# Performance work log

Measured on AMD Instinct MI355X. Metric: run time of the kernel, lower is better.

Reference implementation:

```python
import jax, jax.numpy as jnp
import numpy as np

# Static tree structure: B jets, each a perfect binary tree of depth DEPTH.
B = 64
DEPTH = 12                       # levels 0..DEPTH; level j has B*2**j nodes
N_FEAT = 7
N_HID = 128
LEVEL_SIZES = [B * (1 << j) for j in range(DEPTH + 1)]
OFFSETS = np.concatenate([[0], np.cumsum(LEVEL_SIZES)]).astype(np.int64).tolist()
TOTAL = OFFSETS[-1]              # 524224 nodes
INNER_SIZES = LEVEL_SIZES[:-1]   # all nodes inner except leaf level
INNER_OFF = np.concatenate([[0], np.cumsum(INNER_SIZES)]).astype(np.int64).tolist()


def setup_inputs() -> dict:
    key = jax.random.key(0)
    k_c, k_wu, k_wh = jax.random.split(key, 3)
    contents = jax.random.normal(k_c, (TOTAL, N_FEAT), dtype=jnp.float32)
    # children: per level j < DEPTH, a random pairing (permutation) of level j+1 nodes
    rng = np.random.default_rng(0)
    ch = []
    for j in range(DEPTH):
        perm = rng.permutation(LEVEL_SIZES[j + 1]).astype(np.int32)
        ch.append(perm.reshape(LEVEL_SIZES[j], 2))
    children = jnp.asarray(np.concatenate(ch, axis=0))  # [262080, 2]
    # Learned params (torch nn.Linear: y = x @ W.T + b)
    w_u = jax.random.normal(k_wu, (N_HID, N_FEAT), dtype=jnp.float32) / np.float32(np.sqrt(N_FEAT))
    b_u = jnp.zeros((N_HID,), jnp.float32)
    w_h = jax.random.normal(k_wh, (N_HID, 3 * N_HID), dtype=jnp.float32) / np.float32(np.sqrt(3 * N_HID))
    b_h = jnp.zeros((N_HID,), jnp.float32)
    return {"contents": contents, "children": children,
            "w_u": w_u, "b_u": b_u, "w_h": w_h, "b_h": b_h}


def reference(contents, children, w_u, b_u, w_h, b_h):
    # Bottom-up pass over tree levels (leaves -> root), mirroring the torch loop
    # over levels[::-1]. Perfect binary tree: every non-leaf node is inner.
    emb = None
    for j in range(DEPTH, -1, -1):
        c_j = contents[OFFSETS[j]:OFFSETS[j + 1]]              # [B*2^j, F]
        u = jnp.tanh(c_j @ w_u.T + b_u)                        # [B*2^j, H]
        if j < DEPTH:
            ch_j = children[INNER_OFF[j]:INNER_OFF[j + 1]]     # [B*2^j, 2]
            h_L = emb[ch_j[:, 0]]                              # gather from prev level
            h_R = emb[ch_j[:, 1]]
            emb = jnp.tanh(jnp.concatenate([h_L, h_R, u], axis=1) @ w_h.T + b_h)
        else:
            emb = u  # leaf level: no inner nodes
    return emb.reshape(B, -1)  # root embedding per jet: [B, N_HID]
```

## Files before the change

kernel.cpp:

```cpp
#include <hip/hip_runtime.h>
#include <hip/hip_bf16.h>


#define NF 7
#define NH 128
#define NLEAF 262144
#define XSTR 136
#define XSTR3 392

typedef __bf16 bf16;
typedef __bf16 bf16x8 __attribute__((ext_vector_type(8)));
typedef float floatx16 __attribute__((ext_vector_type(16)));

__device__ __forceinline__ float ftanh(float x){
    float e = __expf(2.0f * x);
    return 1.0f - __fdividef(2.0f, e + 1.0f);
}

__global__ __launch_bounds__(256) void k_leaf(
    const float* __restrict__ contents, const int2* __restrict__ children,
    const float* __restrict__ w_u, const float* __restrict__ b_u,
    const float* __restrict__ w_h,
    unsigned int* __restrict__ embA_u32, unsigned int* __restrict__ usm_u32,
    bf16* __restrict__ wb, int* __restrict__ ids_A, int* __restrict__ ids_B)
{
    const int t = threadIdx.x;
    const int b = blockIdx.x;

    if (b >= 2560){
        if (b < 2564){
            int root = (b - 2560) * 256 + t;
            int* base = ids_A + root * 128;
            const int2* ch4 = children + 960;
            const int2* ch5 = children + 1984;
            const int2* ch6 = children + 4032;
            const int2* ch7 = children + 8128;
            const int2* ch8 = children + 16320;
            const int2* ch9 = children + 32704;
            int l5[2], l6[4], l7[8], l8[16], l9[32];
            { int2 c = ch4[root]; l5[0] = c.x; l5[1] = c.y; }
            #pragma unroll
            for (int k = 0; k < 2; ++k){ int2 c = ch5[l5[k]]; l6[2*k] = c.x; l6[2*k+1] = c.y; }
            #pragma unroll
            for (int k = 0; k < 4; ++k){ int2 c = ch6[l6[k]]; l7[2*k] = c.x; l7[2*k+1] = c.y; }
            #pragma unroll
            for (int k = 0; k < 8; ++k){ int2 c = ch7[l7[k]]; l8[2*k] = c.x; l8[2*k+1] = c.y; }
            #pragma unroll
            for (int k = 0; k < 16; ++k){ int2 c = ch8[l8[k]]; l9[2*k] = c.x; l9[2*k+1] = c.y; }
            base[0] = root;
            base[1] = l5[0]; base[2] = l5[1];
            #pragma unroll
            for (int k = 0; k < 4; ++k)  base[3 + k]  = l6[k];
            #pragma unroll
            for (int k = 0; k < 8; ++k)  base[7 + k]  = l7[k];
            #pragma unroll
            for (int k = 0; k < 16; ++k) base[15 + k] = l8[k];
            #pragma unroll
            for (int k = 0; k < 32; ++k) base[31 + k] = l9[k];
            #pragma unroll
            for (int k = 0; k < 32; ++k){
                int2 c = ch9[l9[k]];
                base[63 + 2*k] = c.x; base[64 + 2*k] = c.y;
            }
        } else if (t < 64){
            int root = t;
            int* base = ids_B + root * 32;
            const int2* ch0 = children;
            const int2* ch1 = children + 64;
            const int2* ch2 = children + 192;
            const int2* ch3 = children + 448;
            int l1[2], l2[4], l3[8];
            { int2 c = ch0[root]; l1[0] = c.x; l1[1] = c.y; }
            #pragma unroll
            for (int k = 0; k < 2; ++k){ int2 c = ch1[l1[k]]; l2[2*k] = c.x; l2[2*k+1] = c.y; }
            #pragma unroll
            for (int k = 0; k < 4; ++k){ int2 c = ch2[l2[k]]; l3[2*k] = c.x; l3[2*k+1] = c.y; }
            base[0] = root;
            base[1] = l1[0]; base[2] = l1[1];
            #pragma unroll
            for (int k = 0; k < 4; ++k) base[3 + k] = l2[k];
            #pragma unroll
            for (int k = 0; k < 8; ++k) base[7 + k] = l3[k];
            #pragma unroll
            for (int k = 0; k < 8; ++k){
                int2 c = ch3[l3[k]];
                base[15 + 2*k] = c.x; base[16 + 2*k] = c.y;
            }
        }
        return;
    }

    __shared__ float csL[128 * 8];
    if (b < 192) wb[b * 256 + t] = (bf16)w_h[b * 256 + t];

    const int leaf = (b < 2048);
    const size_t srow = leaf ? (262080 + (size_t)b * 128) : ((size_t)(b - 2048) * 128);
    unsigned int* dst = leaf ? embA_u32 : usm_u32;
    const size_t drow = leaf ? ((size_t)b * 128) : ((size_t)(b - 2048) * 128);

    if (t < 224){
        float4 v = ((const float4*)(contents + srow * NF))[t];
        int e = t * 4;
        float vv[4] = {v.x, v.y, v.z, v.w};
        #pragma unroll
        for (int r = 0; r < 4; ++r){ int ee = e + r; csL[(ee/7)*8 + (ee%7)] = vv[r]; }
    }
    const int cp = t & 63;
    const int quarter = t >> 6;
    float wu0[NF], wu1[NF];
    const float* w0 = w_u + (size_t)(2 * cp) * NF;
    #pragma unroll
    for (int f = 0; f < NF; ++f){ wu0[f] = w0[f]; wu1[f] = w0[NF + f]; }
    const float bu0 = b_u[2 * cp], bu1 = b_u[2 * cp + 1];
    __syncthreads();
    #pragma unroll 4
    for (int i = 0; i < 32; ++i){
        int node = quarter * 32 + i;
        float4 c0 = *(const float4*)&csL[node * 8];
        float4 c1 = *(const float4*)&csL[node * 8 + 4];
        float a0 = bu0, a1 = bu1;
        a0 = fmaf(c0.x, wu0[0], a0); a1 = fmaf(c0.x, wu1[0], a1);
        a0 = fmaf(c0.y, wu0[1], a0); a1 = fmaf(c0.y, wu1[1], a1);
        a0 = fmaf(c0.z, wu0[2], a0); a1 = fmaf(c0.z, wu1[2], a1);
        a0 = fmaf(c0.w, wu0[3], a0); a1 = fmaf(c0.w, wu1[3], a1);
        a0 = fmaf(c1.x, wu0[4], a0); a1 = fmaf(c1.x, wu1[4], a1);
        a0 = fmaf(c1.y, wu0[5], a0); a1 = fmaf(c1.y, wu1[5], a1);
        a0 = fmaf(c1.z, wu0[6], a0); a1 = fmaf(c1.z, wu1[6], a1);
        union { unsigned int u; bf16 h[2]; } pk;
        pk.h[0] = (bf16)ftanh(a0);
        pk.h[1] = (bf16)ftanh(a1);
        dst[(drow + node) * 64 + cp] = pk.u;
    }
}

__global__ __launch_bounds__(256, 4) void k_inner(
    const int2* __restrict__ children, const float* __restrict__ contents,
    const float* __restrict__ w_u, const float* __restrict__ b_u,
    const bf16* __restrict__ wb, const float* __restrict__ b_h,
    const bf16* __restrict__ emb_next, bf16* __restrict__ out_b)
{
    __shared__ bf16 xs[64 * XSTR];
    __shared__ int2 ch_s[64];
    __shared__ float cs[64 * 8];
    const int t = threadIdx.x;
    const int block0 = blockIdx.x * 64;
    if (t < 64) ch_s[t] = children[block0 + t];
    if (t < 112){
        float4 v = ((const float4*)(contents + (size_t)block0 * NF))[t];
        int e = t * 4;
        float vv[4] = {v.x, v.y, v.z, v.w};
        #pragma unroll
        for (int r = 0; r < 4; ++r){ int ee = e + r; cs[(ee/7)*8 + (ee%7)] = vv[r]; }
    }
    const int cp = t & 63;
    const int quarter = t >> 6;
    float wu0[NF], wu1[NF];
    {
        const float* w0 = w_u + (size_t)(2 * cp) * NF;
        #pragma unroll
        for (int f = 0; f < NF; ++f){ wu0[f] = w0[f]; wu1[f] = w0[NF + f]; }
    }
    const float bu0 = b_u[2 * cp], bu1 = b_u[2 * cp + 1];
    const int lane = t & 63;
    const int ct = t >> 6;
    const int m = lane & 31;
    const int q = lane >> 5;
    floatx16 acc0 = {0,0,0,0,0,0,0,0,0,0,0,0,0,0,0,0};
    floatx16 acc1 = {0,0,0,0,0,0,0,0,0,0,0,0,0,0,0,0};
    const bf16* bq = wb + ((size_t)(ct * 32 + m) * 384 + q * 8);
    #pragma unroll 1
    for (int p = 0; p < 3; ++p){
        __syncthreads();
        if (p < 2){
            #pragma unroll
            for (int r = 0; r < 4; ++r){
                int task = r * 256 + t;
                int i = task >> 4, part = task & 15;
                int row = (p == 0) ? ch_s[i].x : ch_s[i].y;
                uint4 v = *(const uint4*)(emb_next + (size_t)row * NH + part * 8);
                *(uint4*)&xs[i * XSTR + part * 8] = v;
            }
        } else {
            #pragma unroll 4
            for (int i = 0; i < 16; ++i){
                int node = quarter * 16 + i;
                float4 c0 = *(const float4*)&cs[node * 8];
                float4 c1 = *(const float4*)&cs[node * 8 + 4];
                float a0 = bu0, a1 = bu1;
                a0 = fmaf(c0.x, wu0[0], a0); a1 = fmaf(c0.x, wu1[0], a1);
                a0 = fmaf(c0.y, wu0[1], a0); a1 = fmaf(c0.y, wu1[1], a1);
                a0 = fmaf(c0.z, wu0[2], a0); a1 = fmaf(c0.z, wu1[2], a1);
                a0 = fmaf(c0.w, wu0[3], a0); a1 = fmaf(c0.w, wu1[3], a1);
                a0 = fmaf(c1.x, wu0[4], a0); a1 = fmaf(c1.x, wu1[4], a1);
                a0 = fmaf(c1.y, wu0[5], a0); a1 = fmaf(c1.y, wu1[5], a1);
                a0 = fmaf(c1.z, wu0[6], a0); a1 = fmaf(c1.z, wu1[6], a1);
                union { unsigned int u; bf16 h[2]; } pk;
                pk.h[0] = (bf16)ftanh(a0);
                pk.h[1] = (bf16)ftanh(a1);
                ((unsigned int*)xs)[node * (XSTR / 2) + cp] = pk.u;
            }
        }
        bf16x8 bfr[8];
        #pragma unroll
        for (int kk = 0; kk < 8; ++kk)
            bfr[kk] = *(const bf16x8*)(bq + p * 128 + kk * 16);
        __syncthreads();
        const bf16* xa = &xs[m * XSTR + q * 8];
        #pragma unroll
        for (int kk = 0; kk < 8; ++kk){
            bf16x8 a0 = *(const bf16x8*)(xa + kk * 16);
            bf16x8 a1 = *(const bf16x8*)(xa + kk * 16 + 32 * XSTR);
            acc0 = __builtin_amdgcn_mfma_f32_32x32x16_bf16(a0, bfr[kk], acc0, 0, 0, 0);
            acc1 = __builtin_amdgcn_mfma_f32_32x32x16_bf16(a1, bfr[kk], acc1, 0, 0, 0);
        }
    }
    const int colg = ct * 32 + m;
    const float bv = b_h[colg];
    #pragma unroll
    for (int nt = 0; nt < 2; ++nt){
        const floatx16* accp = nt ? &acc1 : &acc0;
        #pragma unroll
        for (int r = 0; r < 16; ++r){
            int row  = (r & 3) + 8 * (r >> 2) + 4 * q;
            int node = block0 + nt * 32 + row;
            out_b[(size_t)node * NH + colg] = (bf16)ftanh((*accp)[r] + bv);
        }
    }
}

__global__ __launch_bounds__(256, 2) void k_tailA(
    const int* __restrict__ ids_A, const bf16* __restrict__ u_small,
    const bf16* __restrict__ wb, const float* __restrict__ b_h,
    const bf16* __restrict__ emb10, bf16* __restrict__ emb4)
{
    __shared__ bf16 xs[32 * XSTR3];
    __shared__ bf16 embL[32 * 136];
    __shared__ int ids[128];
    const int t = threadIdx.x, root = blockIdx.x;
    const int ct = t >> 6, lane = t & 63, m = lane & 31, q = lane >> 5;
    const float bv = b_h[ct * 32 + m];
    if (t < 32) ((uint4*)ids)[t] = ((const uint4*)(ids_A + root * 128))[t];
    __syncthreads();
    const bf16* bq = wb + ((size_t)(ct * 32 + m) * 384 + q * 8);

    #pragma unroll 1
    for (int l = 9; l >= 4; --l){
        const int n = 1 << (l - 4);
        #pragma unroll 1
        for (int r = 0; r < 4; ++r){
            int task = r * 256 + t;
            if (task < n * 32){
                int i = task >> 5, half = (task >> 4) & 1, part = task & 15;
                uint4 v;
                if (l == 9) v = *(const uint4*)(emb10 + (size_t)ids[63 + 2*i + half] * NH + part * 8);
                else        v = *(uint4*)&embL[(2*i + half) * 136 + part * 8];
                *(uint4*)&xs[i * XSTR3 + half * 128 + part * 8] = v;
            }
        }
        #pragma unroll 1
        for (int r = 0; r < 2; ++r){
            int task = r * 256 + t;
            if (task < n * 16){
                int i = task >> 4, part = task & 15;
                size_t row = (size_t)64 * ((1u << l) - 1) + ids[(n - 1) + i];
                *(uint4*)&xs[i * XSTR3 + 256 + part * 8] =
                    *(const uint4*)(u_small + row * NH + part * 8);
            }
        }
        __syncthreads();
        floatx16 accs[3];
        #pragma unroll
        for (int g = 0; g < 3; ++g) accs[g] = (floatx16){0,0,0,0,0,0,0,0,0,0,0,0,0,0,0,0};
        const bf16* xa = &xs[m * XSTR3 + q * 8];
        #pragma unroll
        for (int grp = 0; grp < 3; ++grp){
            bf16x8 bfr[8];
            #pragma unroll
            for (int kk = 0; kk < 8; ++kk)
                bfr[kk] = *(const bf16x8*)(bq + grp * 128 + kk * 16);
            #pragma unroll
            for (int kk = 0; kk < 8; ++kk){
                bf16x8 a0 = *(const bf16x8*)(xa + grp * 128 + kk * 16);
                accs[grp] = __builtin_amdgcn_mfma_f32_32x32x16_bf16(a0, bfr[kk], accs[grp], 0, 0, 0);
            }
        }
        floatx16 acc = accs[0] + accs[1] + accs[2];
        __syncthreads();
        #pragma unroll
        for (int r = 0; r < 16; ++r){
            int row = (r & 3) + 8 * (r >> 2) + 4 * q;
            if (row < n){
                float v = ftanh(acc[r] + bv);
                if (l > 4) embL[row * 136 + ct * 32 + m] = (bf16)v;
                else       emb4[(size_t)root * NH + ct * 32 + m] = (bf16)v;
            }
        }
        __syncthreads();
    }
}

__global__ __launch_bounds__(256, 2) void k_tailB(
    const int* __restrict__ ids_B, const bf16* __restrict__ u_small,
    const bf16* __restrict__ wb, const float* __restrict__ b_h,
    const bf16* __restrict__ emb4, float* __restrict__ out_f)
{
    __shared__ bf16 xs[8 * XSTR3];
    __shared__ bf16 embL[8 * 136];
    __shared__ int ids[32];
    const int t = threadIdx.x, root = blockIdx.x;
    const int ct = t >> 6, lane = t & 63, m = lane & 31, q = lane >> 5;
    const float bv = b_h[ct * 32 + m];
    if (t < 8) ((uint4*)ids)[t] = ((const uint4*)(ids_B + root * 32))[t];
    __syncthreads();
    const bf16* bq = wb + ((size_t)(ct * 32 + m) * 384 + q * 8);

    #pragma unroll 1
    for (int l = 3; l >= 0; --l){
        const int n = 1 << l;
        {
            int task = t;
            if (task < n * 32){
                int i = task >> 5, half = (task >> 4) & 1, part = task & 15;
                uint4 v;
                if (l == 3) v = *(const uint4*)(emb4 + (size_t)ids[15 + 2*i + half] * NH + part * 8);
                else        v = *(uint4*)&embL[(2*i + half) * 136 + part * 8];
                *(uint4*)&xs[i * XSTR3 + half * 128 + part * 8] = v;
            }
            if (task < n * 16){
                int i = task >> 4, part = task & 15;
                size_t row = (size_t)64 * ((1u << l) - 1) + ids[(n - 1) + i];
                *(uint4*)&xs[i * XSTR3 + 256 + part * 8] =
                    *(const uint4*)(u_small + row * NH + part * 8);
            }
        }
        __syncthreads();
        floatx16 accs[3];
        #pragma unroll
        for (int g = 0; g < 3; ++g) accs[g] = (floatx16){0,0,0,0,0,0,0,0,0,0,0,0,0,0,0,0};
        const bf16* xa = &xs[m * XSTR3 + q * 8];
        #pragma unroll
        for (int grp = 0; grp < 3; ++grp){
            bf16x8 bfr[8];
            #pragma unroll
            for (int kk = 0; kk < 8; ++kk)
                bfr[kk] = *(const bf16x8*)(bq + grp * 128 + kk * 16);
            #pragma unroll
            for (int kk = 0; kk < 8; ++kk){
                bf16x8 a0 = *(const bf16x8*)(xa + grp * 128 + kk * 16);
                accs[grp] = __builtin_amdgcn_mfma_f32_32x32x16_bf16(a0, bfr[kk], accs[grp], 0, 0, 0);
            }
        }
        floatx16 acc = accs[0] + accs[1] + accs[2];
        __syncthreads();
        #pragma unroll
        for (int r = 0; r < 16; ++r){
            int row = (r & 3) + 8 * (r >> 2) + 4 * q;
            if (row < n){
                float v = ftanh(acc[r] + bv);
                if (l > 0) embL[row * 136 + ct * 32 + m] = (bf16)v;
                else       out_f[(size_t)root * NH + ct * 32 + m] = v;
            }
        }
        __syncthreads();
    }
}

extern "C" void kernel_launch(void* const* d_in, const int* in_sizes, int n_in,
                              void* d_out, int out_size, void* d_ws, size_t ws_size,
                              hipStream_t stream){
    const float* contents = (const float*)d_in[0];
    const int2*  children = (const int2*)d_in[1];
    const float* w_u      = (const float*)d_in[2];
    const float* b_u      = (const float*)d_in[3];
    const float* w_h      = (const float*)d_in[4];
    const float* b_h      = (const float*)d_in[5];
    float* outf = (float*)d_out;

    bf16* embA    = (bf16*)d_ws;
    bf16* embB    = embA + (size_t)NLEAF * NH;
    bf16* wb      = embB + (size_t)131072 * NH;
    bf16* u_small = wb + (size_t)NH * 384;
    int*  ids_A   = (int*)(u_small + (size_t)65536 * NH);
    int*  ids_B   = ids_A + 1024 * 128;

    hipLaunchKernelGGL(k_leaf, dim3(2565), dim3(256), 0, stream,
                       contents, children, w_u, b_u, w_h,
                       (unsigned int*)embA, (unsigned int*)u_small, wb, ids_A, ids_B);
    hipLaunchKernelGGL(k_inner, dim3(2048), dim3(256), 0, stream,
                       children + 131008, contents + (size_t)131008 * NF,
                       w_u, b_u, wb, b_h, embA, embB);
    hipLaunchKernelGGL(k_inner, dim3(1024), dim3(256), 0, stream,
                       children + 65472, contents + (size_t)65472 * NF,
                       w_u, b_u, wb, b_h, embB, embA);
    hipLaunchKernelGGL(k_tailA, dim3(1024), dim3(256), 0, stream,
                       ids_A, u_small, wb, b_h, embA, embB);
    hipLaunchKernelGGL(k_tailB, dim3(64), dim3(256), 0, stream,
                       ids_B, u_small, wb, b_h, embB, outf);
}
```

Measured before the change: 229.8 us.

## Fuse leaf embedding into level-11 inner kernel, skipping leaf-embedding round trip

The leaf level's tanh(Wu·x) is now computed on the fly inside a new level-11 kernel. Each block gathers its children's leaf contents directly, builds the leaf and node embeddings in shared memory, and runs the MFMA combine. This removes the full leaf-embedding write and re-gather through global memory (about 64 MB of bf16 traffic) and one kernel launch. In exchange, each block reads w_h in fp32 and converts it to bf16 itself rather than using the precomputed wb, which is still built by tail blocks. It also uses more shared memory per block and limits occupancy to two blocks per CU.

After: 240.4 us. 4.6% more time.

```diff
diff --git a/kernel.cpp b/kernel.cpp
--- a/kernel.cpp
+++ b/kernel.cpp
@@ -4,7 +4,6 @@
 
 #define NF 7
 #define NH 128
-#define NLEAF 262144
 #define XSTR 136
 #define XSTR3 392
 
@@ -17,18 +16,58 @@
     return 1.0f - __fdividef(2.0f, e + 1.0f);
 }
 
-__global__ __launch_bounds__(256) void k_leaf(
+__global__ __launch_bounds__(256, 2) void k_lvl11(
     const float* __restrict__ contents, const int2* __restrict__ children,
     const float* __restrict__ w_u, const float* __restrict__ b_u,
-    const float* __restrict__ w_h,
-    unsigned int* __restrict__ embA_u32, unsigned int* __restrict__ usm_u32,
-    bf16* __restrict__ wb, int* __restrict__ ids_A, int* __restrict__ ids_B)
+    const float* __restrict__ w_h, const float* __restrict__ b_h,
+    bf16* __restrict__ emb11,
+    unsigned int* __restrict__ usm_u32, int* __restrict__ ids_A,
+    int* __restrict__ ids_B, bf16* __restrict__ wb)
 {
+    __shared__ bf16 xs[64 * XSTR3];
+    __shared__ float cs2[128 * 8];
+    __shared__ float cs[64 * 8];
+    __shared__ int chS[128];
     const int t = threadIdx.x;
     const int b = blockIdx.x;
 
-    if (b >= 2560){
-        if (b < 2564){
+    if (b >= 2048){
+        if (b < 2560){
+            const size_t srow = (size_t)(b - 2048) * 128;
+            if (t < 224){
+                float4 v = ((const float4*)(contents + srow * NF))[t];
+                int e = t * 4;
+                float vv[4] = {v.x, v.y, v.z, v.w};
+                #pragma unroll
+                for (int r = 0; r < 4; ++r){ int ee = e + r; cs2[(ee/7)*8 + (ee%7)] = vv[r]; }
+            }
+            const int cp = t & 63;
+            const int quarter = t >> 6;
+            float wu0[NF], wu1[NF];
+            const float* w0 = w_u + (size_t)(2 * cp) * NF;
+            #pragma unroll
+            for (int f = 0; f < NF; ++f){ wu0[f] = w0[f]; wu1[f] = w0[NF + f]; }
+            const float bu0 = b_u[2 * cp], bu1 = b_u[2 * cp + 1];
+            __syncthreads();
+            #pragma unroll 4
+            for (int i = 0; i < 32; ++i){
+                int node = quarter * 32 + i;
+                float4 c0 = *(const float4*)&cs2[node * 8];
+                float4 c1 = *(const float4*)&cs2[node * 8 + 4];
+                float a0 = bu0, a1 = bu1;
+                a0 = fmaf(c0.x, wu0[0], a0); a1 = fmaf(c0.x, wu1[0], a1);
+                a0 = fmaf(c0.y, wu0[1], a0); a1 = fmaf(c0.y, wu1[1], a1);
+                a0 = fmaf(c0.z, wu0[2], a0); a1 = fmaf(c0.z, wu1[2], a1);
+                a0 = fmaf(c0.w, wu0[3], a0); a1 = fmaf(c0.w, wu1[3], a1);
+                a0 = fmaf(c1.x, wu0[4], a0); a1 = fmaf(c1.x, wu1[4], a1);
+                a0 = fmaf(c1.y, wu0[5], a0); a1 = fmaf(c1.y, wu1[5], a1);
+                a0 = fmaf(c1.z, wu0[6], a0); a1 = fmaf(c1.z, wu1[6], a1);
+                union { unsigned int u; bf16 h[2]; } pk;
+                pk.h[0] = (bf16)ftanh(a0);
+                pk.h[1] = (bf16)ftanh(a1);
+                usm_u32[(srow + node) * 64 + cp] = pk.u;
+            }
+        } else if (b < 2564){
             int root = (b - 2560) * 256 + t;
             int* base = ids_A + root * 128;
             const int2* ch4 = children + 960;
@@ -62,62 +101,78 @@
                 int2 c = ch9[l9[k]];
                 base[63 + 2*k] = c.x; base[64 + 2*k] = c.y;
             }
-        } else if (t < 64){
-            int root = t;
-            int* base = ids_B + root * 32;
-            const int2* ch0 = children;
-            const int2* ch1 = children + 64;
-            const int2* ch2 = children + 192;
-            const int2* ch3 = children + 448;
-            int l1[2], l2[4], l3[8];
-            { int2 c = ch0[root]; l1[0] = c.x; l1[1] = c.y; }
-            #pragma unroll
-            for (int k = 0; k < 2; ++k){ int2 c = ch1[l1[k]]; l2[2*k] = c.x; l2[2*k+1] = c.y; }
-            #pragma unroll
-            for (int k = 0; k < 4; ++k){ int2 c = ch2[l2[k]]; l3[2*k] = c.x; l3[2*k+1] = c.y; }
-            base[0] = root;
-            base[1] = l1[0]; base[2] = l1[1];
-            #pragma unroll
-            for (int k = 0; k < 4; ++k) base[3 + k] = l2[k];
-            #pragma unroll
-            for (int k = 0; k < 8; ++k) base[7 + k] = l3[k];
-            #pragma unroll
-            for (int k = 0; k < 8; ++k){
-                int2 c = ch3[l3[k]];
-                base[15 + 2*k] = c.x; base[16 + 2*k] = c.y;
-            }
+        } else if (b == 2564){
+            if (t < 64){
+                int root = t;
+                int* base = ids_B + root * 32;
+                const int2* ch0 = children;
+                const int2* ch1 = children + 64;
+                const int2* ch2 = children + 192;
+                const int2* ch3 = children + 448;
+                int l1[2], l2[4], l3[8];
+                { int2 c = ch0[root]; l1[0] = c.x; l1[1] = c.y; }
+                #pragma unroll
+                for (int k = 0; k < 2; ++k){ int2 c = ch1[l1[k]]; l2[2*k] = c.x; l2[2*k+1] = c.y; }
+                #pragma unroll
+                for (int k = 0; k < 4; ++k){ int2 c = ch2[l2[k]]; l3[2*k] = c.x; l3[2*k+1] = c.y; }
+                base[0] = root;
+                base[1] = l1[0]; base[2] = l1[1];
+                #pragma unroll
+                for (int k = 0; k < 4; ++k) base[3 + k] = l2[k];
+                #pragma unroll
+                for (int k = 0; k < 8; ++k) base[7 + k] = l3[k];
+                #pragma unroll
+                for (int k = 0; k < 8; ++k){
+                    int2 c = ch3[l3[k]];
+                    base[15 + 2*k] = c.x; base[16 + 2*k] = c.y;
+                }
+            }
+        } else {
+            int idx = (b - 2565) * 256 + t;
+            wb[idx] = (bf16)w_h[idx];
         }
         return;
     }
 
-    __shared__ float csL[128 * 8];
-    if (b < 192) wb[b * 256 + t] = (bf16)w_h[b * 256 + t];
-
-    const int leaf = (b < 2048);
-    const size_t srow = leaf ? (262080 + (size_t)b * 128) : ((size_t)(b - 2048) * 128);
-    unsigned int* dst = leaf ? embA_u32 : usm_u32;
-    const size_t drow = leaf ? ((size_t)b * 128) : ((size_t)(b - 2048) * 128);
-
-    if (t < 224){
-        float4 v = ((const float4*)(contents + srow * NF))[t];
+    const int node0 = b * 64;
+    const int2* ch11 = children + 131008;
+    const float* cont11 = contents + (size_t)131008 * NF;
+    const float* contL  = contents + (size_t)262080 * NF;
+
+    if (t < 64){ int2 c = ch11[node0 + t]; chS[2*t] = c.x; chS[2*t + 1] = c.y; }
+    if (t < 112){
+        float4 v = ((const float4*)(cont11 + (size_t)node0 * NF))[t];
         int e = t * 4;
         float vv[4] = {v.x, v.y, v.z, v.w};
         #pragma unroll
-        for (int r = 0; r < 4; ++r){ int ee = e + r; csL[(ee/7)*8 + (ee%7)] = vv[r]; }
-    }
+        for (int r = 0; r < 4; ++r){ int ee = e + r; cs[(ee/7)*8 + (ee%7)] = vv[r]; }
+    }
+
     const int cp = t & 63;
     const int quarter = t >> 6;
     float wu0[NF], wu1[NF];
-    const float* w0 = w_u + (size_t)(2 * cp) * NF;
-    #pragma unroll
-    for (int f = 0; f < NF; ++f){ wu0[f] = w0[f]; wu1[f] = w0[NF + f]; }
+    {
+        const float* w0 = w_u + (size_t)(2 * cp) * NF;
+        #pragma unroll
+        for (int f = 0; f < NF; ++f){ wu0[f] = w0[f]; wu1[f] = w0[NF + f]; }
+    }
     const float bu0 = b_u[2 * cp], bu1 = b_u[2 * cp + 1];
+    unsigned int* xs32 = (unsigned int*)xs;
+
     __syncthreads();
+
+    float c7[NF];
+    if (t < 128){
+        const float* src = contL + (size_t)chS[t] * NF;
+        #pragma unroll
+        for (int f = 0; f < NF; ++f) c7[f] = src[f];
+    }
+
     #pragma unroll 4
-    for (int i = 0; i < 32; ++i){
-        int node = quarter * 32 + i;
-        float4 c0 = *(const float4*)&csL[node * 8];
-        float4 c1 = *(const float4*)&csL[node * 8 + 4];
+    for (int k = 0; k < 16; ++k){
+        int i = quarter * 16 + k;
+        float4 c0 = *(const float4*)&cs[i * 8];
+        float4 c1 = *(const float4*)&cs[i * 8 + 4];
         float a0 = bu0, a1 = bu1;
         a0 = fmaf(c0.x, wu0[0], a0); a1 = fmaf(c0.x, wu1[0], a1);
         a0 = fmaf(c0.y, wu0[1], a0); a1 = fmaf(c0.y, wu1[1], a1);
@@ -129,7 +184,77 @@
         union { unsigned int u; bf16 h[2]; } pk;
         pk.h[0] = (bf16)ftanh(a0);
         pk.h[1] = (bf16)ftanh(a1);
-        dst[(drow + node) * 64 + cp] = pk.u;
+        xs32[i * (XSTR3 / 2) + 128 + cp] = pk.u;
+    }
+
+    if (t < 128){
+        #pragma unroll
+        for (int f = 0; f < NF; ++f) cs2[t * 8 + f] = c7[f];
+    }
+    __syncthreads();
+
+    #pragma unroll 4
+    for (int k = 0; k < 32; ++k){
+        int c = quarter * 32 + k;
+        float4 c0 = *(const float4*)&cs2[c * 8];
+        float4 c1 = *(const float4*)&cs2[c * 8 + 4];
+        float a0 = bu0, a1 = bu1;
+        a0 = fmaf(c0.x, wu0[0], a0); a1 = fmaf(c0.x, wu1[0], a1);
+        a0 = fmaf(c0.y, wu0[1], a0); a1 = fmaf(c0.y, wu1[1], a1);
+        a0 = fmaf(c0.z, wu0[2], a0); a1 = fmaf(c0.z, wu1[2], a1);
+        a0 = fmaf(c0.w, wu0[3], a0); a1 = fmaf(c0.w, wu1[3], a1);
+        a0 = fmaf(c1.x, wu0[4], a0); a1 = fmaf(c1.x, wu1[4], a1);
+        a0 = fmaf(c1.y, wu0[5], a0); a1 = fmaf(c1.y, wu1[5], a1);
+        a0 = fmaf(c1.z, wu0[6], a0); a1 = fmaf(c1.z, wu1[6], a1);
+        union { unsigned int u; bf16 h[2]; } pk;
+        pk.h[0] = (bf16)ftanh(a0);
+        pk.h[1] = (bf16)ftanh(a1);
+        xs32[(c >> 1) * (XSTR3 / 2) + (c & 1) * 64 + cp] = pk.u;
+    }
+    __syncthreads();
+
+    const int lane = t & 63;
+    const int ct = t >> 6;
+    const int m = lane & 31;
+    const int q = lane >> 5;
+    floatx16 acc0 = {0,0,0,0,0,0,0,0,0,0,0,0,0,0,0,0};
+    floatx16 acc1 = {0,0,0,0,0,0,0,0,0,0,0,0,0,0,0,0};
+    const float* bqf = w_h + ((size_t)(ct * 32 + m) * 384 + q * 8);
+    const bf16* xa = &xs[m * XSTR3 + q * 8];
+    #pragma unroll
+    for (int grp = 0; grp < 3; ++grp){
+        bf16x8 bfr[8];
+        #pragma unroll
+        for (int kk = 0; kk < 8; ++kk){
+            float4 f0 = *(const float4*)(bqf + grp * 128 + kk * 16);
+            float4 f1 = *(const float4*)(bqf + grp * 128 + kk * 16 + 4);
+            union { bf16x8 v; bf16 h[8]; } u8;
+            u8.h[0] = (bf16)f0.x; u8.h[1] = (bf16)f0.y;
+            u8.h[2] = (bf16)f0.z; u8.h[3] = (bf16)f0.w;
+            u8.h[4] = (bf16)f1.x; u8.h[5] = (bf16)f1.y;
+            u8.h[6] = (bf16)f1.z; u8.h[7] = (bf16)f1.w;
+            bfr[kk] = u8.v;
+        }
+        #pragma unroll
+        for (int kk = 0; kk < 8; ++kk){
+            bf16x8 a0 = *(const bf16x8*)(xa + grp * 128 + kk * 16);
+            bf16x8 a1 = *(const bf16x8*)(xa + grp * 128 + kk * 16 + 32 * XSTR3);
+            acc0 = __builtin_amdgcn_mfma_f32_32x32x16_bf16(a0, bfr[kk], acc0, 0, 0, 0);
+            acc1 = __builtin_amdgcn_mfma_f32_32x32x16_bf16(a1, bfr[kk], acc1, 0, 0, 0);
+        }
+    }
+
+    const int colg = ct * 32 + m;
+    const float bv = b_h[colg];
+    #pragma unroll
+    for (int nt = 0; nt < 2; ++nt){
+        const floatx16* accp = nt ? &acc1 : &acc0;
+        #pragma unroll
+        for (int r = 0; r < 16; ++r){
+            int row  = (r & 3) + 8 * (r >> 2) + 4 * q;
+            int node = node0 + nt * 32 + row;
+            emb11[(size_t)node * NH + colg] = (bf16)ftanh((*accp)[r] + bv);
+        }
     }
 }
 
@@ -377,18 +502,15 @@
     float* outf = (float*)d_out;
 
     bf16* embA    = (bf16*)d_ws;
-    bf16* embB    = embA + (size_t)NLEAF * NH;
+    bf16* embB    = embA + (size_t)65536 * NH;
     bf16* wb      = embB + (size_t)131072 * NH;
     bf16* u_small = wb + (size_t)NH * 384;
     int*  ids_A   = (int*)(u_small + (size_t)65536 * NH);
     int*  ids_B   = ids_A + 1024 * 128;
 
-    hipLaunchKernelGGL(k_leaf, dim3(2565), dim3(256), 0, stream,
-                       contents, children, w_u, b_u, w_h,
-                       (unsigned int*)embA, (unsigned int*)u_small, wb, ids_A, ids_B);
-    hipLaunchKernelGGL(k_inner, dim3(2048), dim3(256), 0, stream,
-                       children + 131008, contents + (size_t)131008 * NF,
-                       w_u, b_u, wb, b_h, embA, embB);
+    hipLaunchKernelGGL(k_lvl11, dim3(2757), dim3(256), 0, stream,
+                       contents, children, w_u, b_u, w_h, b_h,
+                       embB, (unsigned int*)u_small, ids_A, ids_B, wb);
     hipLaunchKernelGGL(k_inner, dim3(1024), dim3(256), 0, stream,
                        children + 65472, contents + (size_t)65472 * NF,
                        w_u, b_u, wb, b_h, embB, embA);
```

## Fuse leaf embedding into level-11 kernel via MFMA instead of materializing leaves

Applied to the files above, without the earlier changes.

The leaf-level embeddings (262144 nodes) are no longer written to global memory. The new level-11 kernel gathers each node's two children's raw features, computes their tanh(W_u x + b) with a small bf16 MFMA (bias folded into an augmented input column), and feeds them straight into the level-11 combine GEMM through shared memory. The prep kernel now handles only the levels 0-10 u-vectors, index tables and weight conversion. This removes a large global write and reread of leaf embeddings, at the cost of bf16 rounding in the leaf projection and extra shared memory per block.

New measurement: 223.0 us. 1.03x faster.

```diff
diff --git a/kernel.cpp b/kernel.cpp
--- a/kernel.cpp
+++ b/kernel.cpp
@@ -4,7 +4,6 @@
 
 #define NF 7
 #define NH 128
-#define NLEAF 262144
 #define XSTR 136
 #define XSTR3 392
 
@@ -17,19 +16,56 @@
     return 1.0f - __fdividef(2.0f, e + 1.0f);
 }
 
-__global__ __launch_bounds__(256) void k_leaf(
+__global__ __launch_bounds__(256) void k_prep(
     const float* __restrict__ contents, const int2* __restrict__ children,
     const float* __restrict__ w_u, const float* __restrict__ b_u,
     const float* __restrict__ w_h,
-    unsigned int* __restrict__ embA_u32, unsigned int* __restrict__ usm_u32,
-    bf16* __restrict__ wb, int* __restrict__ ids_A, int* __restrict__ ids_B)
+    unsigned int* __restrict__ usm_u32, int* __restrict__ ids_A,
+    int* __restrict__ ids_B, bf16* __restrict__ wb, bf16* __restrict__ w_ub)
 {
+    __shared__ float csL[128 * 8];
     const int t = threadIdx.x;
     const int b = blockIdx.x;
 
-    if (b >= 2560){
-        if (b < 2564){
-            int root = (b - 2560) * 256 + t;
+    if (b >= 512){
+        if (b == 512){
+            if (t < 64){
+                int root = t;
+                int* base = ids_B + root * 32;
+                const int2* ch0 = children;
+                const int2* ch1 = children + 64;
+                const int2* ch2 = children + 192;
+                const int2* ch3 = children + 448;
+                int l1[2], l2[4], l3[8];
+                { int2 c = ch0[root]; l1[0] = c.x; l1[1] = c.y; }
+                #pragma unroll
+                for (int k = 0; k < 2; ++k){ int2 c = ch1[l1[k]]; l2[2*k] = c.x; l2[2*k+1] = c.y; }
+                #pragma unroll
+                for (int k = 0; k < 4; ++k){ int2 c = ch2[l2[k]]; l3[2*k] = c.x; l3[2*k+1] = c.y; }
+                base[0] = root;
+                base[1] = l1[0]; base[2] = l1[1];
+                #pragma unroll
+                for (int k = 0; k < 4; ++k) base[3 + k] = l2[k];
+                #pragma unroll
+                for (int k = 0; k < 8; ++k) base[7 + k] = l3[k];
+                #pragma unroll
+                for (int k = 0; k < 8; ++k){
+                    int2 c = ch3[l3[k]];
+                    base[15 + 2*k] = c.x; base[16 + 2*k] = c.y;
+                }
+            } else if (t < 192){
+                int col = t - 64;
+                union { uint4 u4[2]; bf16 h[16]; } row;
+                #pragma unroll
+                for (int f = 0; f < NF; ++f) row.h[f] = (bf16)w_u[col * NF + f];
+                row.h[7] = (bf16)b_u[col];
+                #pragma unroll
+                for (int k = 8; k < 16; ++k) row.h[k] = (bf16)0.0f;
+                *(uint4*)&w_ub[col * 16]     = row.u4[0];
+                *(uint4*)&w_ub[col * 16 + 8] = row.u4[1];
+            }
+        } else if (b < 517){
+            int root = (b - 513) * 256 + t;
             int* base = ids_A + root * 128;
             const int2* ch4 = children + 960;
             const int2* ch5 = children + 1984;
@@ -62,42 +98,14 @@
                 int2 c = ch9[l9[k]];
                 base[63 + 2*k] = c.x; base[64 + 2*k] = c.y;
             }
-        } else if (t < 64){
-            int root = t;
-            int* base = ids_B + root * 32;
-            const int2* ch0 = children;
-            const int2* ch1 = children + 64;
-            const int2* ch2 = children + 192;
-            const int2* ch3 = children + 448;
-            int l1[2], l2[4], l3[8];
-            { int2 c = ch0[root]; l1[0] = c.x; l1[1] = c.y; }
-            #pragma unroll
-            for (int k = 0; k < 2; ++k){ int2 c = ch1[l1[k]]; l2[2*k] = c.x; l2[2*k+1] = c.y; }
-            #pragma unroll
-            for (int k = 0; k < 4; ++k){ int2 c = ch2[l2[k]]; l3[2*k] = c.x; l3[2*k+1] = c.y; }
-            base[0] = root;
-            base[1] = l1[0]; base[2] = l1[1];
-            #pragma unroll
-            for (int k = 0; k < 4; ++k) base[3 + k] = l2[k];
-            #pragma unroll
-            for (int k = 0; k < 8; ++k) base[7 + k] = l3[k];
-            #pragma unroll
-            for (int k = 0; k < 8; ++k){
-                int2 c = ch3[l3[k]];
-                base[15 + 2*k] = c.x; base[16 + 2*k] = c.y;
-            }
+        } else {
+            int idx = (b - 517) * 256 + t;
+            wb[idx] = (bf16)w_h[idx];
         }
         return;
     }
 
-    __shared__ float csL[128 * 8];
-    if (b < 192) wb[b * 256 + t] = (bf16)w_h[b * 256 + t];
-
-    const int leaf = (b < 2048);
-    const size_t srow = leaf ? (262080 + (size_t)b * 128) : ((size_t)(b - 2048) * 128);
-    unsigned int* dst = leaf ? embA_u32 : usm_u32;
-    const size_t drow = leaf ? ((size_t)b * 128) : ((size_t)(b - 2048) * 128);
-
+    const size_t srow = (size_t)b * 128;
     if (t < 224){
         float4 v = ((const float4*)(contents + srow * NF))[t];
         int e = t * 4;
@@ -129,7 +137,97 @@
         union { unsigned int u; bf16 h[2]; } pk;
         pk.h[0] = (bf16)ftanh(a0);
         pk.h[1] = (bf16)ftanh(a1);
-        dst[(drow + node) * 64 + cp] = pk.u;
+        usm_u32[(srow + node) * 64 + cp] = pk.u;
+    }
+}
+
+__global__ __launch_bounds__(256, 2) void k_lvl11(
+    const float* __restrict__ contents, const int2* __restrict__ children,
+    const bf16* __restrict__ w_ub, const bf16* __restrict__ wb,
+    const float* __restrict__ b_h, bf16* __restrict__ emb11)
+{
+    __shared__ bf16 xs[64 * XSTR3];
+    __shared__ bf16 ca[192 * 16];
+    __shared__ int chS[128];
+    const int t = threadIdx.x;
+    const int node0 = blockIdx.x * 64;
+    const int2* ch11 = children + 131008;
+    const float* cont11 = contents + (size_t)131008 * NF;
+    const float* contL  = contents + (size_t)262080 * NF;
+
+    if (t < 64){ int2 c = ch11[node0 + t]; chS[2*t] = c.x; chS[2*t + 1] = c.y; }
+    __syncthreads();
+
+    if (t < 192){
+        const float* src = (t < 128) ? (contL + (size_t)chS[t] * NF)
+                                     : (cont11 + (size_t)(node0 + t - 128) * NF);
+        union { uint4 u4[2]; bf16 h[16]; } row;
+        #pragma unroll
+        for (int f = 0; f < NF; ++f) row.h[f] = (bf16)src[f];
+        row.h[7] = (bf16)1.0f;
+        #pragma unroll
+        for (int k = 8; k < 16; ++k) row.h[k] = (bf16)0.0f;
+        *(uint4*)&ca[t * 16]     = row.u4[0];
+        *(uint4*)&ca[t * 16 + 8] = row.u4[1];
+    }
+
+    const int lane = t & 63;
+    const int ct = t >> 6;
+    const int m = lane & 31;
+    const int q = lane >> 5;
+    const int colg = ct * 32 + m;
+    const bf16x8 bu = *(const bf16x8*)(w_ub + (size_t)colg * 16 + q * 8);
+    __syncthreads();
+
+    #pragma unroll
+    for (int tile = 0; tile < 6; ++tile){
+        bf16x8 a = *(const bf16x8*)&ca[(tile * 32 + m) * 16 + q * 8];
+        floatx16 acc = {0,0,0,0,0,0,0,0,0,0,0,0,0,0,0,0};
+        acc = __builtin_amdgcn_mfma_f32_32x32x16_bf16(a, bu, acc, 0, 0, 0);
+        #pragma unroll
+        for (int r = 0; r < 16; ++r){
+            int row = (r & 3) + 8 * (r >> 2) + 4 * q;
+            bf16 hv = (bf16)ftanh(acc[r]);
+            if (tile < 4){
+                int c = tile * 32 + row;
+                xs[(c >> 1) * XSTR3 + (c & 1) * 128 + colg] = hv;
+            } else {
+                int i = (tile - 4) * 32 + row;
+                xs[i * XSTR3 + 256 + colg] = hv;
+            }
+        }
+    }
+    __syncthreads();
+
+    floatx16 acc0 = {0,0,0,0,0,0,0,0,0,0,0,0,0,0,0,0};
+    floatx16 acc1 = {0,0,0,0,0,0,0,0,0,0,0,0,0,0,0,0};
+    const bf16* bq = wb + (size_t)colg * 384 + q * 8;
+    const bf16* xa = &xs[m * XSTR3 + q * 8];
+    #pragma unroll
+    for (int grp = 0; grp < 3; ++grp){
+        bf16x8 bfr[8];
+        #pragma unroll
+        for (int kk = 0; kk < 8; ++kk)
+            bfr[kk] = *(const bf16x8*)(bq + grp * 128 + kk * 16);
+        #pragma unroll
+        for (int kk = 0; kk < 8; ++kk){
+            bf16x8 a0 = *(const bf16x8*)(xa + grp * 128 + kk * 16);
+            bf16x8 a1 = *(const bf16x8*)(xa + grp * 128 + kk * 16 + 32 * XSTR3);
+            acc0 = __builtin_amdgcn_mfma_f32_32x32x16_bf16(a0, bfr[kk], acc0, 0, 0, 0);
+            acc1 = __builtin_amdgcn_mfma_f32_32x32x16_bf16(a1, bfr[kk], acc1, 0, 0, 0);
+        }
+    }
+
+    const float bv = b_h[colg];
+    #pragma unroll
+    for (int nt = 0; nt < 2; ++nt){
+        const floatx16* accp = nt ? &acc1 : &acc0;
+        #pragma unroll
+        for (int r = 0; r < 16; ++r){
+            int row  = (r & 3) + 8 * (r >> 2) + 4 * q;
+            int node = node0 + nt * 32 + row;
+            emb11[(size_t)node * NH + colg] = (bf16)ftanh((*accp)[r] + bv);
+        }
     }
 }
 
@@ -377,18 +475,18 @@
     float* outf = (float*)d_out;
 
     bf16* embA    = (bf16*)d_ws;
-    bf16* embB    = embA + (size_t)NLEAF * NH;
+    bf16* embB    = embA + (size_t)65536 * NH;
     bf16* wb      = embB + (size_t)131072 * NH;
     bf16* u_small = wb + (size_t)NH * 384;
     int*  ids_A   = (int*)(u_small + (size_t)65536 * NH);
     int*  ids_B   = ids_A + 1024 * 128;
-
-    hipLaunchKernelGGL(k_leaf, dim3(2565), dim3(256), 0, stream,
+    bf16* w_ub    = (bf16*)(ids_B + 64 * 32);
+
+    hipLaunchKernelGGL(k_prep, dim3(709), dim3(256), 0, stream,
                        contents, children, w_u, b_u, w_h,
-                       (unsigned int*)embA, (unsigned int*)u_small, wb, ids_A, ids_B);
-    hipLaunchKernelGGL(k_inner, dim3(2048), dim3(256), 0, stream,
-                       children + 131008, contents + (size_t)131008 * NF,
-                       w_u, b_u, wb, b_h, embA, embB);
+                       (unsigned int*)u_small, ids_A, ids_B, wb, w_ub);
+    hipLaunchKernelGGL(k_lvl11, dim3(2048), dim3(256), 0, stream,
+                       contents, children, w_ub, wb, b_h, embB);
     hipLaunchKernelGGL(k_inner, dim3(1024), dim3(256), 0, stream,
                        children + 65472, contents + (size_t)65472 * NF,
                        w_u, b_u, wb, b_h, embB, embA);
```
